# Optimization experiments

Measured on AMD Instinct MI355X. Metric: run time of the kernel, lower is better.

## Reference

```python
import jax, jax.numpy as jnp
import numpy as np

B, P, E, H, U = 64, 256, 256, 8, 6
HD = E // H            # head_dim = 32
TOPK = 32
DFF = 4 * E
EPS_LN = 1e-5
EPS_RMS = 1.1920929e-07  # torch.finfo(float32).eps (RMSNorm default eps)
NEG = -1e9


def setup_inputs() -> dict:
    key = jax.random.key(0)
    ks = jax.random.split(key, 10)
    s = 0.02
    f32 = jnp.float32
    return {
        "x": jax.random.normal(ks[0], (B, P, E), f32),
        "u": jax.random.normal(ks[1], (B, U, P, P), f32),
        "norm1_w": jnp.ones((E,), f32),
        "norm1_b": jnp.zeros((E,), f32),
        "wq": jax.random.normal(ks[2], (E, E), f32) * s,
        "wk": jax.random.normal(ks[3], (E, E), f32) * s,
        "wv": jax.random.normal(ks[4], (E, E), f32) * s,
        "wo": jax.random.normal(ks[5], (E, E), f32) * s,
        "bo": jnp.zeros((E,), f32),
        "uw": jax.random.normal(ks[6], (H, U), f32) * s,  # 1x1 Conv2d(u_embed->H)
        "ub": jnp.zeros((H,), f32),
        "norm2_w": jnp.ones((E,), f32),
        "norm2_b": jnp.zeros((E,), f32),
        "rms_w": jnp.ones((E,), f32),
        "w1": jax.random.normal(ks[7], (E, DFF), f32) * s,
        "b1": jnp.zeros((DFF,), f32),
        "w2": jax.random.normal(ks[8], (DFF, E), f32) * s,
        "b2": jnp.zeros((E,), f32),
    }


def _layernorm(x, w, b):
    m = jnp.mean(x, axis=-1, keepdims=True)
    v = jnp.mean(jnp.square(x - m), axis=-1, keepdims=True)
    return (x - m) * jax.lax.rsqrt(v + EPS_LN) * w + b


def reference(x, u, norm1_w, norm1_b, wq, wk, wv, wo, bo, uw, ub,
              norm2_w, norm2_b, rms_w, w1, b1, w2, b2):
    xn = _layernorm(x, norm1_w, norm1_b)
    # projections -> [B, H, P, HD]
    q = (xn @ wq).reshape(B, P, H, HD).transpose(0, 2, 1, 3)
    k = (xn @ wk).reshape(B, P, H, HD).transpose(0, 2, 1, 3)
    v = (xn @ wv).reshape(B, P, H, HD).transpose(0, 2, 1, 3)
    scores = jnp.einsum('bhqd,bhkd->bhqk', q, k) * (HD ** -0.5)

    # 1x1 conv bias over pairwise features: [B, U, P, P] -> [B, H, P, P]
    uh = jnp.einsum('bupq,hu->bhpq', u, uw) + ub[None, :, None, None]

    # top-k sparse mask from edge importance (sum of |bias| over heads)
    imp = jnp.abs(uh).sum(axis=1)                    # [B, P, P]
    kk = min(TOPK, P - 1)
    _, idx = jax.lax.top_k(imp, kk)                  # [B, P, kk]
    mask = jnp.zeros((B, P, P), dtype=bool).at[
        jnp.arange(B)[:, None, None],
        jnp.arange(P)[None, :, None],
        idx,
    ].set(True)
    uh = jnp.where(mask[:, None, :, :], uh, NEG)

    attn = jax.nn.softmax(scores + uh, axis=-1)
    attn = jnp.nan_to_num(attn, nan=0.0)

    ctx = jnp.einsum('bhqk,bhkd->bhqd', attn, v)
    ctx = ctx.transpose(0, 2, 1, 3).reshape(B, P, E)
    attn_out = ctx @ wo + bo

    h = _layernorm(attn_out, norm2_w, norm2_b) + x
    hn = h * jax.lax.rsqrt(jnp.mean(h * h, axis=-1, keepdims=True) + EPS_RMS) * rms_w
    z = jax.nn.silu(hn @ w1 + b1) @ w2 + b2
    return z + h, attn
```

## Files before the change

### kernel.cpp

```cpp
#include <hip/hip_runtime.h>
#include <hip/hip_bf16.h>

typedef unsigned short u16;
typedef unsigned long long u64;
typedef __attribute__((ext_vector_type(8))) short short8;
typedef __attribute__((ext_vector_type(4))) float f32x4;

#define NB 64
#define NP 256
#define NE 256
#define NH 8
#define NHD 32
#define NU 6
#define NDFF 1024
#define NM (NB*NP)

__device__ __forceinline__ u16 f2bf(float f) {
  unsigned u = __float_as_uint(f);
  unsigned r = 0x7fffu + ((u >> 16) & 1u);
  return (u16)((u + r) >> 16);
}
__device__ __forceinline__ float bf2f(u16 v) {
  unsigned u = ((unsigned)v) << 16;
  return __uint_as_float(u);
}

__device__ __forceinline__ void gl_lds16(const u16* g, u16* l) {
  __builtin_amdgcn_global_load_lds(
      (const __attribute__((address_space(1))) unsigned int*)g,
      (__attribute__((address_space(3))) unsigned int*)l, 16, 0, 0);
}

__global__ __launch_bounds__(256) void k_prep(
    const float* __restrict__ wq, const float* __restrict__ wk, const float* __restrict__ wv,
    const float* __restrict__ wo, const float* __restrict__ w1, const float* __restrict__ w2,
    u16* __restrict__ wqkvT, u16* __restrict__ woT, u16* __restrict__ w1T, u16* __restrict__ w2T) {
  int tid = blockIdx.x * 256 + threadIdx.x;
  int stride = gridDim.x * 256;
  for (int i = tid; i < 768 * 256; i += stride) {
    int n = i >> 8, kk = i & 255;
    const float* s = (n < 256) ? wq : ((n < 512) ? wk : wv);
    wqkvT[i] = f2bf(s[kk * 256 + (n & 255)]);
  }
  for (int i = tid; i < 256 * 256; i += stride)  { int n = i >> 8,  kk = i & 255;  woT[i] = f2bf(wo[kk * 256 + n]); }
  for (int i = tid; i < 1024 * 256; i += stride) { int n = i >> 8,  kk = i & 255;  w1T[i] = f2bf(w1[kk * 1024 + n]); }
  for (int i = tid; i < 256 * 1024; i += stride) { int n = i >> 10, kk = i & 1023; w2T[i] = f2bf(w2[kk * 256 + n]); }
}

__global__ __launch_bounds__(256) void k_ln1(
    const float* __restrict__ x, const float* __restrict__ w, const float* __restrict__ b,
    u16* __restrict__ xn) {
  int row = blockIdx.x * 4 + (threadIdx.x >> 6);
  int lane = threadIdx.x & 63;
  const float* xr = x + (size_t)row * NE;
  float4 v = *(const float4*)(xr + lane * 4);
  float s = v.x + v.y + v.z + v.w;
  #pragma unroll
  for (int o = 32; o; o >>= 1) s += __shfl_xor(s, o);
  float mean = s * (1.f / 256.f);
  float d0 = v.x - mean, d1 = v.y - mean, d2 = v.z - mean, d3 = v.w - mean;
  float q = d0*d0 + d1*d1 + d2*d2 + d3*d3;
  #pragma unroll
  for (int o = 32; o; o >>= 1) q += __shfl_xor(q, o);
  float r = rsqrtf(q * (1.f / 256.f) + 1e-5f);
  int c = lane * 4;
  ushort4 o4;
  o4.x = f2bf(d0 * r * w[c+0] + b[c+0]);
  o4.y = f2bf(d1 * r * w[c+1] + b[c+1]);
  o4.z = f2bf(d2 * r * w[c+2] + b[c+2]);
  o4.w = f2bf(d3 * r * w[c+3] + b[c+3]);
  *(ushort4*)(xn + (size_t)row * NE + c) = o4;
}

template<class Epi>
__global__ __launch_bounds__(256, 4) void k_gemm128(
    const u16* __restrict__ A, const u16* __restrict__ BT, int K, Epi epi) {
  __shared__ __align__(16) u16 As[128 * 32];
  __shared__ __align__(16) u16 Bs[128 * 32];
  const int t = threadIdx.x;
  const int m0 = blockIdx.x * 128, n0 = blockIdx.y * 128;
  const int lane = t & 63, wv = t >> 6;
  const int fr = lane & 15, fg = lane >> 4;
  const int wm = (wv >> 1) * 64, wn = (wv & 1) * 64;
  const u16* Ap = A + (size_t)(m0 + (t >> 2)) * K + (t & 3) * 8;
  const u16* Bp = BT + (size_t)(n0 + (t >> 2)) * K + (t & 3) * 8;
  u16* lA = As + wv * 512;
  u16* lB = Bs + wv * 512;
  f32x4 acc[4][4] = {};
  for (int k0 = 0; k0 < K; k0 += 32) {
    __syncthreads();
    gl_lds16(Ap + k0, lA);
    gl_lds16(Ap + k0 + (size_t)64 * K, lA + 2048);
    gl_lds16(Bp + k0, lB);
    gl_lds16(Bp + k0 + (size_t)64 * K, lB + 2048);
    __syncthreads();
    short8 a[4], b[4];
    #pragma unroll
    for (int i = 0; i < 4; i++) a[i] = *(const short8*)(As + (wm + i * 16 + fr) * 32 + fg * 8);
    #pragma unroll
    for (int j = 0; j < 4; j++) b[j] = *(const short8*)(Bs + (wn + j * 16 + fr) * 32 + fg * 8);
    #pragma unroll
    for (int i = 0; i < 4; i++)
      #pragma unroll
      for (int j = 0; j < 4; j++)
        acc[i][j] = __builtin_amdgcn_mfma_f32_16x16x32_bf16(a[i], b[j], acc[i][j], 0, 0, 0);
  }
  #pragma unroll
  for (int i = 0; i < 4; i++)
    #pragma unroll
    for (int j = 0; j < 4; j++)
      #pragma unroll
      for (int jj = 0; jj < 4; jj++)
        epi(m0 + wm + i * 16 + fg * 4 + jj, n0 + wn + j * 16 + fr, acc[i][j][jj]);
}

struct EpiQKV {
  u16 *q, *k, *vT;
  __device__ __forceinline__ void operator()(int m, int n, float v) const {
    int b = m >> 8, p = m & 255;
    int h = (n >> 5) & 7, d = n & 31;
    u16 bv = f2bf(v);
    if (n < 256)       q [(((size_t)(b*NH + h)) * NP + p) * NHD + d] = bv;
    else if (n < 512)  k [(((size_t)(b*NH + h)) * NP + p) * NHD + d] = bv;
    else               vT[(((size_t)(b*NH + h)) * NHD + d) * NP + p] = bv;
  }
};
struct EpiWo {
  const float* bo; float* ao;
  __device__ __forceinline__ void operator()(int m, int n, float v) const {
    ao[(size_t)m * NE + n] = v + bo[n];
  }
};
struct EpiFFN1 {
  const float* b1; u16* tb;
  __device__ __forceinline__ void operator()(int m, int n, float v) const {
    float s = v + b1[n];
    tb[(size_t)m * NDFF + n] = f2bf(s / (1.f + __expf(-s)));
  }
};
struct EpiFFN2 {
  const float* b2; const float* hb; float* out0;
  __device__ __forceinline__ void operator()(int m, int n, float v) const {
    out0[(size_t)m * NE + n] = v + b2[n] + hb[(size_t)m * NE + n];
  }
};

__global__ __launch_bounds__(512, 4) void k_fattn(
    const float* __restrict__ u, const float* __restrict__ uw, const float* __restrict__ ub,
    const u16* __restrict__ qb, const u16* __restrict__ kb, const u16* __restrict__ vTb,
    float* __restrict__ attn, u16* __restrict__ ctx) {
  __shared__ __align__(16) u16 bias[NH * 16 * 256];
  const int b = blockIdx.x >> 4;
  const int r0 = (blockIdx.x & 15) << 4;
  const int w = threadIdx.x >> 6;
  const int lane = threadIdx.x & 63;
  const int fr = lane & 15, fg = lane >> 4;
  const u16 NEGBF = f2bf(-1e9f);

  for (int rr = 0; rr < 2; rr++) {
    const int p = r0 + 2 * w + rr;
    const float* up = u + ((size_t)b * NU * NP + p) * NP + lane * 4;
    double uh[NH][4];
    #pragma unroll
    for (int h = 0; h < NH; h++) {
      double bb = (double)ub[h];
      uh[h][0] = bb; uh[h][1] = bb; uh[h][2] = bb; uh[h][3] = bb;
    }
    #pragma unroll
    for (int uu = 0; uu < NU; uu++) {
      float4 uv = *(const float4*)(up + (size_t)uu * (NP * NP));
      #pragma unroll
      for (int h = 0; h < NH; h++) {
        double ww = (double)uw[h * NU + uu];
        uh[h][0] += ww * (double)uv.x;
        uh[h][1] += ww * (double)uv.y;
        uh[h][2] += ww * (double)uv.z;
        uh[h][3] += ww * (double)uv.w;
      }
    }
    u64 ib[4];
    #pragma unroll
    for (int i = 0; i < 4; i++) {
      double imp = 0.0;
      #pragma unroll
      for (int h = 0; h < NH; h++) imp += fabs(uh[h][i]);
      ib[i] = (u64)__double_as_longlong(imp);
    }
    u64 res = 0;
    for (int bit = 62; bit >= 0; --bit) {
      u64 cand = res | (1ull << bit);
      int c = __popcll(__ballot(ib[0] >= cand)) + __popcll(__ballot(ib[1] >= cand))
            + __popcll(__ballot(ib[2] >= cand)) + __popcll(__ballot(ib[3] >= cand));
      if (c >= 32) res = cand;
    }
    const int rl = 2 * w + rr;
    #pragma unroll
    for (int h = 0; h < NH; h++) {
      ushort4 o;
      o.x = (ib[0] >= res) ? f2bf((float)uh[h][0]) : NEGBF;
      o.y = (ib[1] >= res) ? f2bf((float)uh[h][1]) : NEGBF;
      o.z = (ib[2] >= res) ? f2bf((float)uh[h][2]) : NEGBF;
      o.w = (ib[3] >= res) ? f2bf((float)uh[h][3]) : NEGBF;
      *(ushort4*)(bias + (h * 16 + rl) * 256 + lane * 4) = o;
    }
  }
  __syncthreads();

  const size_t bh = (size_t)b * NH + w;
  const u16* qp = qb + (bh * NP + r0) * NHD;
  short8 af = *(const short8*)(qp + fr * NHD + fg * 8);
  const u16* kp = kb + bh * NP * NHD;
  const float scale = 0.17677669529663687f;
  f32x4 sc[16];
  #pragma unroll
  for (int nb = 0; nb < 16; nb++) {
    short8 bfr = *(const short8*)(kp + (nb * 16 + fr) * NHD + fg * 8);
    f32x4 z = {0.f, 0.f, 0.f, 0.f};
    z = __builtin_amdgcn_mfma_f32_16x16x32_bf16(af, bfr, z, 0, 0, 0);
    #pragma unroll
    for (int jj = 0; jj < 4; jj++)
      sc[nb][jj] = z[jj] * scale + bf2f(bias[(w * 16 + fg * 4 + jj) * 256 + nb * 16 + fr]);
  }
  float mx[4] = {-1e30f, -1e30f, -1e30f, -1e30f};
  #pragma unroll
  for (int nb = 0; nb < 16; nb++)
    #pragma unroll
    for (int jj = 0; jj < 4; jj++) mx[jj] = fmaxf(mx[jj], sc[nb][jj]);
  #pragma unroll
  for (int o = 1; o < 16; o <<= 1)
    #pragma unroll
    for (int jj = 0; jj < 4; jj++) mx[jj] = fmaxf(mx[jj], __shfl_xor(mx[jj], o));
  float sum[4] = {0.f, 0.f, 0.f, 0.f};
  #pragma unroll
  for (int nb = 0; nb < 16; nb++)
    #pragma unroll
    for (int jj = 0; jj < 4; jj++) {
      sc[nb][jj] = __expf(sc[nb][jj] - mx[jj]);
      sum[jj] += sc[nb][jj];
    }
  #pragma unroll
  for (int o = 1; o < 16; o <<= 1)
    #pragma unroll
    for (int jj = 0; jj < 4; jj++) sum[jj] += __shfl_xor(sum[jj], o);
  float inv[4];
  #pragma unroll
  for (int jj = 0; jj < 4; jj++) inv[jj] = 1.f / sum[jj];

  float* ap = attn + (bh * NP + r0 + fg * 4) * NP;
  u16* ps = bias + w * 4096;
  #pragma unroll
  for (int nb = 0; nb < 16; nb++)
    #pragma unroll
    for (int jj = 0; jj < 4; jj++) {
      float e = sc[nb][jj] * inv[jj];
      ap[jj * 256 + nb * 16 + fr] = e;
      int row = fg * 4 + jj, col = nb * 16 + fr;
      ps[row * 256 + ((((col >> 3) ^ (row & 7)) << 3) | (col & 7))] = f2bf(e);
    }

  const u16* vp = vTb + bh * NHD * NP;
  f32x4 c0 = {0.f, 0.f, 0.f, 0.f}, c1 = {0.f, 0.f, 0.f, 0.f};
  #pragma unroll
  for (int kk = 0; kk < 8; kk++) {
    short8 pa = *(const short8*)(ps + fr * 256 + (((kk * 4 + fg) ^ (fr & 7)) << 3));
    short8 v0 = *(const short8*)(vp + fr * NP + kk * 32 + fg * 8);
    short8 v1 = *(const short8*)(vp + (16 + fr) * NP + kk * 32 + fg * 8);
    c0 = __builtin_amdgcn_mfma_f32_16x16x32_bf16(pa, v0, c0, 0, 0, 0);
    c1 = __builtin_amdgcn_mfma_f32_16x16x32_bf16(pa, v1, c1, 0, 0, 0);
  }
  #pragma unroll
  for (int jj = 0; jj < 4; jj++) {
    int prow = r0 + fg * 4 + jj;
    u16* crow = ctx + ((size_t)(b * NP + prow)) * NE + w * NHD;
    crow[fr]      = f2bf(c0[jj]);
    crow[16 + fr] = f2bf(c1[jj]);
  }
}

__global__ __launch_bounds__(256) void k_ln2rms(
    const float* __restrict__ ao, const float* __restrict__ x,
    const float* __restrict__ w, const float* __restrict__ b, const float* __restrict__ rw,
    float* __restrict__ hbuf, u16* __restrict__ hn) {
  int row = blockIdx.x * 4 + (threadIdx.x >> 6);
  int lane = threadIdx.x & 63;
  float4 v = *(const float4*)(ao + (size_t)row * NE + lane * 4);
  float s = v.x + v.y + v.z + v.w;
  #pragma unroll
  for (int o = 32; o; o >>= 1) s += __shfl_xor(s, o);
  float mean = s * (1.f / 256.f);
  float d0 = v.x - mean, d1 = v.y - mean, d2 = v.z - mean, d3 = v.w - mean;
  float q = d0*d0 + d1*d1 + d2*d2 + d3*d3;
  #pragma unroll
  for (int o = 32; o; o >>= 1) q += __shfl_xor(q, o);
  float r = rsqrtf(q * (1.f / 256.f) + 1e-5f);
  float4 xv = *(const float4*)(x + (size_t)row * NE + lane * 4);
  int c = lane * 4;
  float h0 = d0 * r * w[c+0] + b[c+0] + xv.x;
  float h1 = d1 * r * w[c+1] + b[c+1] + xv.y;
  float h2 = d2 * r * w[c+2] + b[c+2] + xv.z;
  float h3 = d3 * r * w[c+3] + b[c+3] + xv.w;
  *(float4*)(hbuf + (size_t)row * NE + c) = make_float4(h0, h1, h2, h3);
  float ss = h0*h0 + h1*h1 + h2*h2 + h3*h3;
  #pragma unroll
  for (int o = 32; o; o >>= 1) ss += __shfl_xor(ss, o);
  float rm = rsqrtf(ss * (1.f / 256.f) + 1.1920929e-07f);
  ushort4 o4;
  o4.x = f2bf(h0 * rm * rw[c+0]);
  o4.y = f2bf(h1 * rm * rw[c+1]);
  o4.z = f2bf(h2 * rm * rw[c+2]);
  o4.w = f2bf(h3 * rm * rw[c+3]);
  *(ushort4*)(hn + (size_t)row * NE + c) = o4;
}

extern "C" void kernel_launch(void* const* d_in, const int* in_sizes, int n_in,
                              void* d_out, int out_size, void* d_ws, size_t ws_size,
                              hipStream_t stream) {
  (void)in_sizes; (void)n_in; (void)out_size; (void)ws_size;
  const float* x    = (const float*)d_in[0];
  const float* u    = (const float*)d_in[1];
  const float* n1w  = (const float*)d_in[2];
  const float* n1b  = (const float*)d_in[3];
  const float* wq   = (const float*)d_in[4];
  const float* wk   = (const float*)d_in[5];
  const float* wv   = (const float*)d_in[6];
  const float* wo   = (const float*)d_in[7];
  const float* bo   = (const float*)d_in[8];
  const float* uw   = (const float*)d_in[9];
  const float* ub   = (const float*)d_in[10];
  const float* n2w  = (const float*)d_in[11];
  const float* n2b  = (const float*)d_in[12];
  const float* rmsw = (const float*)d_in[13];
  const float* w1   = (const float*)d_in[14];
  const float* b1   = (const float*)d_in[15];
  const float* w2   = (const float*)d_in[16];
  const float* b2   = (const float*)d_in[17];
  float* out0 = (float*)d_out;
  float* attn = out0 + (size_t)NM * NE;
  char* ws = (char*)d_ws;
  u16* wqkvT = (u16*)(ws + 0x000000);
  u16* woT   = (u16*)(ws + 0x060000);
  u16* w1T   = (u16*)(ws + 0x080000);
  u16* w2T   = (u16*)(ws + 0x100000);
  u16* qb    = (u16*)(ws + 0x200000);
  u16* kb    = (u16*)(ws + 0xA00000);
  u16* vTb   = (u16*)(ws + 0x1200000);
  u16* xn    = (u16*)(ws + 0x1A00000);
  u16* ctx   = (u16*)(ws + 0x2200000);
  float* ao  = (float*)(ws + 0x2A00000);
  float* hb  = (float*)(ws + 0x3A00000);
  u16* hn    = (u16*)(ws + 0x4A00000);
  u16* tb    = (u16*)(ws + 0x200000);

  k_prep<<<dim3(256), dim3(256), 0, stream>>>(wq, wk, wv, wo, w1, w2, wqkvT, woT, w1T, w2T);
  k_ln1<<<dim3(NM/4), dim3(256), 0, stream>>>(x, n1w, n1b, xn);
  k_gemm128<<<dim3(NM/128, 768/128), dim3(256), 0, stream>>>(xn, wqkvT, NE, EpiQKV{qb, kb, vTb});
  k_fattn<<<dim3(NB*16), dim3(512), 0, stream>>>(u, uw, ub, qb, kb, vTb, attn, ctx);
  k_gemm128<<<dim3(NM/128, NE/128), dim3(256), 0, stream>>>(ctx, woT, NE, EpiWo{bo, ao});
  k_ln2rms<<<dim3(NM/4), dim3(256), 0, stream>>>(ao, x, n2w, n2b, rmsw, hb, hn);
  k_gemm128<<<dim3(NM/128, NDFF/128), dim3(256), 0, stream>>>(hn, w1T, NE, EpiFFN1{b1, tb});
  k_gemm128<<<dim3(NM/128, NE/128), dim3(256), 0, stream>>>(tb, w2T, NDFF, EpiFFN2{b2, hb, out0});
}
```

Before: 480.7 us.

## Tile weight transpose, swizzle GEMM LDS, and restructure fused attention softmax

The weight-prep kernel now transposes through a 32x33 shared-memory tile so both its reads and writes are coalesced. The GEMM LDS layout gets an XOR swizzle to reduce bank conflicts. The attention kernel streams the u projection per head without keeping all heads in double registers, and recomputes QK scores in a second pass instead of holding 16 score fragments. Exponentials are staged as bf16 in LDS and written to attn as coalesced float4 rows, with normalisation applied to ctx afterwards. Launch bounds, block-to-batch mapping and the prep grid size also change; the extra QK MFMA pass and bf16-rounded exponentials trade a little compute and precision for lower register pressure.

```diff
diff --git a/kernel.cpp b/kernel.cpp
--- a/kernel.cpp
+++ b/kernel.cpp
@@ -4,6 +4,7 @@
 typedef unsigned short u16;
 typedef unsigned long long u64;
 typedef __attribute__((ext_vector_type(8))) short short8;
+typedef __attribute__((ext_vector_type(4))) short s16x4;
 typedef __attribute__((ext_vector_type(4))) float f32x4;
 
 #define NB 64
@@ -21,8 +22,7 @@
   return (u16)((u + r) >> 16);
 }
 __device__ __forceinline__ float bf2f(u16 v) {
-  unsigned u = ((unsigned)v) << 16;
-  return __uint_as_float(u);
+  return __uint_as_float(((unsigned)v) << 16);
 }
 
 __device__ __forceinline__ void gl_lds16(const u16* g, u16* l) {
@@ -35,16 +35,22 @@
     const float* __restrict__ wq, const float* __restrict__ wk, const float* __restrict__ wv,
     const float* __restrict__ wo, const float* __restrict__ w1, const float* __restrict__ w2,
     u16* __restrict__ wqkvT, u16* __restrict__ woT, u16* __restrict__ w1T, u16* __restrict__ w2T) {
-  int tid = blockIdx.x * 256 + threadIdx.x;
-  int stride = gridDim.x * 256;
-  for (int i = tid; i < 768 * 256; i += stride) {
-    int n = i >> 8, kk = i & 255;
-    const float* s = (n < 256) ? wq : ((n < 512) ? wk : wv);
-    wqkvT[i] = f2bf(s[kk * 256 + (n & 255)]);
-  }
-  for (int i = tid; i < 256 * 256; i += stride)  { int n = i >> 8,  kk = i & 255;  woT[i] = f2bf(wo[kk * 256 + n]); }
-  for (int i = tid; i < 1024 * 256; i += stride) { int n = i >> 8,  kk = i & 255;  w1T[i] = f2bf(w1[kk * 1024 + n]); }
-  for (int i = tid; i < 256 * 1024; i += stride) { int n = i >> 10, kk = i & 1023; w2T[i] = f2bf(w2[kk * 256 + n]); }
+  __shared__ float tile[32][33];
+  int bid = blockIdx.x;
+  const float* src; u16* dst; int R, C, tr, tc;
+  if (bid < 192)      { int m = bid >> 6, t = bid & 63; src = m==0?wq:(m==1?wk:wv); dst = wqkvT + m*256*256; R=256; C=256;  tr=t>>3; tc=t&7;  }
+  else if (bid < 256) { int t = bid-192; src=wo; dst=woT; R=256;  C=256;  tr=t>>3; tc=t&7;  }
+  else if (bid < 512) { int t = bid-256; src=w1; dst=w1T; R=256;  C=1024; tr=t>>5; tc=t&31; }
+  else                { int t = bid-512; src=w2; dst=w2T; R=1024; C=256;  tr=t>>3; tc=t&7;  }
+  int r0 = tr*32, c0 = tc*32;
+  int rr = threadIdx.x >> 5, cc = threadIdx.x & 31;
+  #pragma unroll
+  for (int p = 0; p < 4; p++)
+    tile[rr + p*8][cc] = src[(size_t)(r0 + rr + p*8) * C + c0 + cc];
+  __syncthreads();
+  #pragma unroll
+  for (int p = 0; p < 4; p++)
+    dst[(size_t)(c0 + rr + p*8) * R + r0 + cc] = f2bf(tile[cc][rr + p*8]);
 }
 
 __global__ __launch_bounds__(256) void k_ln1(
@@ -52,8 +58,7 @@
     u16* __restrict__ xn) {
   int row = blockIdx.x * 4 + (threadIdx.x >> 6);
   int lane = threadIdx.x & 63;
-  const float* xr = x + (size_t)row * NE;
-  float4 v = *(const float4*)(xr + lane * 4);
+  float4 v = *(const float4*)(x + (size_t)row * NE + lane * 4);
   float s = v.x + v.y + v.z + v.w;
   #pragma unroll
   for (int o = 32; o; o >>= 1) s += __shfl_xor(s, o);
@@ -82,8 +87,10 @@
   const int lane = t & 63, wv = t >> 6;
   const int fr = lane & 15, fg = lane >> 4;
   const int wm = (wv >> 1) * 64, wn = (wv & 1) * 64;
-  const u16* Ap = A + (size_t)(m0 + (t >> 2)) * K + (t & 3) * 8;
-  const u16* Bp = BT + (size_t)(n0 + (t >> 2)) * K + (t & 3) * 8;
+  const int row = t >> 2;
+  const int gs = (t & 3) ^ ((row >> 1) & 3);
+  const u16* Ap = A + (size_t)(m0 + row) * K + gs * 8;
+  const u16* Bp = BT + (size_t)(n0 + row) * K + gs * 8;
   u16* lA = As + wv * 512;
   u16* lB = Bs + wv * 512;
   f32x4 acc[4][4] = {};
@@ -96,9 +103,15 @@
     __syncthreads();
     short8 a[4], b[4];
     #pragma unroll
-    for (int i = 0; i < 4; i++) a[i] = *(const short8*)(As + (wm + i * 16 + fr) * 32 + fg * 8);
-    #pragma unroll
-    for (int j = 0; j < 4; j++) b[j] = *(const short8*)(Bs + (wn + j * 16 + fr) * 32 + fg * 8);
+    for (int i = 0; i < 4; i++) {
+      int ra = wm + i * 16 + fr;
+      a[i] = *(const short8*)(As + ra * 32 + ((fg ^ ((ra >> 1) & 3)) << 3));
+    }
+    #pragma unroll
+    for (int j = 0; j < 4; j++) {
+      int rb = wn + j * 16 + fr;
+      b[j] = *(const short8*)(Bs + rb * 32 + ((fg ^ ((rb >> 1) & 3)) << 3));
+    }
     #pragma unroll
     for (int i = 0; i < 4; i++)
       #pragma unroll
@@ -145,13 +158,14 @@
   }
 };
 
-__global__ __launch_bounds__(512, 4) void k_fattn(
+__global__ __launch_bounds__(512, 2) void k_fattn(
     const float* __restrict__ u, const float* __restrict__ uw, const float* __restrict__ ub,
     const u16* __restrict__ qb, const u16* __restrict__ kb, const u16* __restrict__ vTb,
     float* __restrict__ attn, u16* __restrict__ ctx) {
   __shared__ __align__(16) u16 bias[NH * 16 * 256];
-  const int b = blockIdx.x >> 4;
-  const int r0 = (blockIdx.x & 15) << 4;
+  const int i0 = blockIdx.x;
+  const int b = (i0 & 7) * 8 + ((i0 >> 3) & 7);
+  const int r0 = (i0 >> 6) << 4;
   const int w = threadIdx.x >> 6;
   const int lane = threadIdx.x & 63;
   const int fr = lane & 15, fg = lane >> 4;
@@ -159,49 +173,50 @@
 
   for (int rr = 0; rr < 2; rr++) {
     const int p = r0 + 2 * w + rr;
+    const int rl = 2 * w + rr;
     const float* up = u + ((size_t)b * NU * NP + p) * NP + lane * 4;
-    double uh[NH][4];
+    float4 uv[NU];
+    #pragma unroll
+    for (int uu = 0; uu < NU; uu++) uv[uu] = *(const float4*)(up + (size_t)uu * NP * NP);
+    double imp[4] = {0.0, 0.0, 0.0, 0.0};
     #pragma unroll
     for (int h = 0; h < NH; h++) {
-      double bb = (double)ub[h];
-      uh[h][0] = bb; uh[h][1] = bb; uh[h][2] = bb; uh[h][3] = bb;
-    }
-    #pragma unroll
-    for (int uu = 0; uu < NU; uu++) {
-      float4 uv = *(const float4*)(up + (size_t)uu * (NP * NP));
+      double s0 = (double)ub[h], s1 = s0, s2 = s0, s3 = s0;
       #pragma unroll
-      for (int h = 0; h < NH; h++) {
+      for (int uu = 0; uu < NU; uu++) {
         double ww = (double)uw[h * NU + uu];
-        uh[h][0] += ww * (double)uv.x;
-        uh[h][1] += ww * (double)uv.y;
-        uh[h][2] += ww * (double)uv.z;
-        uh[h][3] += ww * (double)uv.w;
+        s0 += ww * (double)uv[uu].x;
+        s1 += ww * (double)uv[uu].y;
+        s2 += ww * (double)uv[uu].z;
+        s3 += ww * (double)uv[uu].w;
       }
-    }
-    u64 ib[4];
-    #pragma unroll
-    for (int i = 0; i < 4; i++) {
-      double imp = 0.0;
-      #pragma unroll
-      for (int h = 0; h < NH; h++) imp += fabs(uh[h][i]);
-      ib[i] = (u64)__double_as_longlong(imp);
-    }
+      imp[0] += fabs(s0); imp[1] += fabs(s1); imp[2] += fabs(s2); imp[3] += fabs(s3);
+      ushort4 o;
+      o.x = f2bf((float)s0); o.y = f2bf((float)s1);
+      o.z = f2bf((float)s2); o.w = f2bf((float)s3);
+      *(ushort4*)(bias + (h * 16 + rl) * 256 + lane * 4) = o;
+    }
+    u64 ib0 = (u64)__double_as_longlong(imp[0]);
+    u64 ib1 = (u64)__double_as_longlong(imp[1]);
+    u64 ib2 = (u64)__double_as_longlong(imp[2]);
+    u64 ib3 = (u64)__double_as_longlong(imp[3]);
     u64 res = 0;
     for (int bit = 62; bit >= 0; --bit) {
       u64 cand = res | (1ull << bit);
-      int c = __popcll(__ballot(ib[0] >= cand)) + __popcll(__ballot(ib[1] >= cand))
-            + __popcll(__ballot(ib[2] >= cand)) + __popcll(__ballot(ib[3] >= cand));
-      if (c >= 32) res = cand;
-    }
-    const int rl = 2 * w + rr;
+      int cnt = __popcll(__ballot(ib0 >= cand)) + __popcll(__ballot(ib1 >= cand))
+              + __popcll(__ballot(ib2 >= cand)) + __popcll(__ballot(ib3 >= cand));
+      if (cnt >= 32) res = cand;
+    }
+    bool k0 = ib0 >= res, k1 = ib1 >= res, k2 = ib2 >= res, k3 = ib3 >= res;
     #pragma unroll
     for (int h = 0; h < NH; h++) {
-      ushort4 o;
-      o.x = (ib[0] >= res) ? f2bf((float)uh[h][0]) : NEGBF;
-      o.y = (ib[1] >= res) ? f2bf((float)uh[h][1]) : NEGBF;
-      o.z = (ib[2] >= res) ? f2bf((float)uh[h][2]) : NEGBF;
-      o.w = (ib[3] >= res) ? f2bf((float)uh[h][3]) : NEGBF;
-      *(ushort4*)(bias + (h * 16 + rl) * 256 + lane * 4) = o;
+      ushort4* pp = (ushort4*)(bias + (h * 16 + rl) * 256 + lane * 4);
+      ushort4 v = *pp;
+      if (!k0) v.x = NEGBF;
+      if (!k1) v.y = NEGBF;
+      if (!k2) v.z = NEGBF;
+      if (!k3) v.w = NEGBF;
+      *pp = v;
     }
   }
   __syncthreads();
@@ -210,8 +225,10 @@
   const u16* qp = qb + (bh * NP + r0) * NHD;
   short8 af = *(const short8*)(qp + fr * NHD + fg * 8);
   const u16* kp = kb + bh * NP * NHD;
+  u16* ps = bias + w * 4096;
   const float scale = 0.17677669529663687f;
-  f32x4 sc[16];
+
+  float mx[4] = {-3e38f, -3e38f, -3e38f, -3e38f};
   #pragma unroll
   for (int nb = 0; nb < 16; nb++) {
     short8 bfr = *(const short8*)(kp + (nb * 16 + fr) * NHD + fg * 8);
@@ -219,25 +236,27 @@
     z = __builtin_amdgcn_mfma_f32_16x16x32_bf16(af, bfr, z, 0, 0, 0);
     #pragma unroll
     for (int jj = 0; jj < 4; jj++)
-      sc[nb][jj] = z[jj] * scale + bf2f(bias[(w * 16 + fg * 4 + jj) * 256 + nb * 16 + fr]);
-  }
-  float mx[4] = {-1e30f, -1e30f, -1e30f, -1e30f};
-  #pragma unroll
-  for (int nb = 0; nb < 16; nb++)
-    #pragma unroll
-    for (int jj = 0; jj < 4; jj++) mx[jj] = fmaxf(mx[jj], sc[nb][jj]);
+      mx[jj] = fmaxf(mx[jj], z[jj] * scale + bf2f(ps[(fg * 4 + jj) * 256 + nb * 16 + fr]));
+  }
   #pragma unroll
   for (int o = 1; o < 16; o <<= 1)
     #pragma unroll
     for (int jj = 0; jj < 4; jj++) mx[jj] = fmaxf(mx[jj], __shfl_xor(mx[jj], o));
+
   float sum[4] = {0.f, 0.f, 0.f, 0.f};
   #pragma unroll
-  for (int nb = 0; nb < 16; nb++)
+  for (int nb = 0; nb < 16; nb++) {
+    short8 bfr = *(const short8*)(kp + (nb * 16 + fr) * NHD + fg * 8);
+    f32x4 z = {0.f, 0.f, 0.f, 0.f};
+    z = __builtin_amdgcn_mfma_f32_16x16x32_bf16(af, bfr, z, 0, 0, 0);
     #pragma unroll
     for (int jj = 0; jj < 4; jj++) {
-      sc[nb][jj] = __expf(sc[nb][jj] - mx[jj]);
-      sum[jj] += sc[nb][jj];
-    }
+      int idx = (fg * 4 + jj) * 256 + nb * 16 + fr;
+      float e = __expf(z[jj] * scale + bf2f(ps[idx]) - mx[jj]);
+      sum[jj] += e;
+      ps[idx] = f2bf(e);
+    }
+  }
   #pragma unroll
   for (int o = 1; o < 16; o <<= 1)
     #pragma unroll
@@ -246,17 +265,24 @@
   #pragma unroll
   for (int jj = 0; jj < 4; jj++) inv[jj] = 1.f / sum[jj];
 
-  float* ap = attn + (bh * NP + r0 + fg * 4) * NP;
-  u16* ps = bias + w * 4096;
-  #pragma unroll
-  for (int nb = 0; nb < 16; nb++)
-    #pragma unroll
-    for (int jj = 0; jj < 4; jj++) {
-      float e = sc[nb][jj] * inv[jj];
-      ap[jj * 256 + nb * 16 + fr] = e;
-      int row = fg * 4 + jj, col = nb * 16 + fr;
-      ps[row * 256 + ((((col >> 3) ^ (row & 7)) << 3) | (col & 7))] = f2bf(e);
-    }
+  s16x4 rowv[16];
+  #pragma unroll
+  for (int i = 0; i < 16; i++) rowv[i] = *(const s16x4*)(ps + i * 256 + lane * 4);
+  float* ab = attn + (bh * NP + r0) * NP;
+  #pragma unroll
+  for (int i = 0; i < 16; i++) {
+    float iv = __shfl(inv[i & 3], (i >> 2) << 4);
+    float4 o;
+    o.x = bf2f((u16)rowv[i][0]) * iv;
+    o.y = bf2f((u16)rowv[i][1]) * iv;
+    o.z = bf2f((u16)rowv[i][2]) * iv;
+    o.w = bf2f((u16)rowv[i][3]) * iv;
+    *(float4*)(ab + i * NP + lane * 4) = o;
+  }
+  const int g = lane >> 1, sub = lane & 1;
+  #pragma unroll
+  for (int i = 0; i < 16; i++)
+    *(s16x4*)(ps + i * 256 + ((g ^ (i & 7)) << 3) + sub * 4) = rowv[i];
 
   const u16* vp = vTb + bh * NHD * NP;
   f32x4 c0 = {0.f, 0.f, 0.f, 0.f}, c1 = {0.f, 0.f, 0.f, 0.f};
@@ -272,8 +298,8 @@
   for (int jj = 0; jj < 4; jj++) {
     int prow = r0 + fg * 4 + jj;
     u16* crow = ctx + ((size_t)(b * NP + prow)) * NE + w * NHD;
-    crow[fr]      = f2bf(c0[jj]);
-    crow[16 + fr] = f2bf(c1[jj]);
+    crow[fr]      = f2bf(c0[jj] * inv[jj]);
+    crow[16 + fr] = f2bf(c1[jj] * inv[jj]);
   }
 }
 
@@ -351,7 +377,7 @@
   u16* hn    = (u16*)(ws + 0x4A00000);
   u16* tb    = (u16*)(ws + 0x200000);
 
-  k_prep<<<dim3(256), dim3(256), 0, stream>>>(wq, wk, wv, wo, w1, w2, wqkvT, woT, w1T, w2T);
+  k_prep<<<dim3(768), dim3(256), 0, stream>>>(wq, wk, wv, wo, w1, w2, wqkvT, woT, w1T, w2T);
   k_ln1<<<dim3(NM/4), dim3(256), 0, stream>>>(x, n1w, n1b, xn);
   k_gemm128<<<dim3(NM/128, 768/128), dim3(256), 0, stream>>>(xn, wqkvT, NE, EpiQKV{qb, kb, vTb});
   k_fattn<<<dim3(NB*16), dim3(512), 0, stream>>>(u, uw, ub, qb, kb, vTb, attn, ctx);
```

Result: faster. 423.0 us (-12.0%).
